# Performance work log

Measured on AMD Instinct MI355X. Metric: run time of the kernel, lower is better.

Reference implementation:

```python
import jax, jax.numpy as jnp
import numpy as np

H = 2048          # hidden_size
I = 1408          # intermediate_size
E = 8             # num_experts
K = 2             # top_k
T = 8192          # tokens


def setup_inputs() -> dict:
    key = jax.random.key(0)
    ks = jax.random.split(key, 7)
    s = 0.02
    return {
        "x": jax.random.normal(ks[0], (T, H), dtype=jnp.float32),
        "w_router": jax.random.normal(ks[1], (H, E), dtype=jnp.float32) * s,
        "w_gate_up": jax.random.normal(ks[2], (E, H, 2 * I), dtype=jnp.float32) * s,
        "w_down": jax.random.normal(ks[3], (E, I, H), dtype=jnp.float32) * s,
        "w_shared_gate_up": jax.random.normal(ks[4], (H, 2 * I), dtype=jnp.float32) * s,
        "w_shared_down": jax.random.normal(ks[5], (I, H), dtype=jnp.float32) * s,
        "w_shared_gate": jax.random.normal(ks[6], (H, 1), dtype=jnp.float32) * s,
    }


def _swiglu_mlp(x, w_gate_up, w_down):
    gu = x @ w_gate_up                      # [T, 2I]
    g, u = jnp.split(gu, 2, axis=-1)
    return (jax.nn.silu(g) * u) @ w_down    # [T, H]


def reference(x, w_router, w_gate_up, w_down, w_shared_gate_up, w_shared_down, w_shared_gate):
    # Router: top-k over logits, softmax over the selected k logits
    logits = x @ w_router                              # [T, E]
    top_vals, top_idx = jax.lax.top_k(logits, K)       # [T, K]
    probs = jax.nn.softmax(top_vals, axis=-1)          # [T, K]

    out = jnp.zeros_like(x)
    for e in range(E):
        sel = (top_idx == e)                           # [T, K] (at most one True per row)
        w_e = jnp.sum(jnp.where(sel, probs, 0.0), axis=-1)  # [T]
        mask = sel.any(axis=-1)                        # [T]
        # Original scales the INPUT by the routing weight before the expert MLP
        xin = x * w_e[:, None]
        o = _swiglu_mlp(xin, w_gate_up[e], w_down[e])
        out = out + jnp.where(mask[:, None], o, 0.0)

    # Shared expert with sigmoid gate
    shared = _swiglu_mlp(x, w_shared_gate_up, w_shared_down)   # [T, H]
    gate = jax.nn.sigmoid(x @ w_shared_gate)                   # [T, 1]
    return out + gate * shared
```

## Files before the change

kernel.cpp:

```cpp
#include <hip/hip_runtime.h>
#include <math.h>

#define H 2048
#define IDIM 1408
#define TWO_I 2816
#define NE 8
#define NTOK 8192
#define BK 32

typedef float f32x4 __attribute__((ext_vector_type(4)));
typedef short bf16x8 __attribute__((ext_vector_type(8)));

#define CNT_OFF   0
#define OFFS_OFF  64
#define BIDX_OFF  1024
#define BW_OFF    (BIDX_OFF + NE*NTOK*4)
#define GATE_OFF  (BW_OFF + NE*NTOK*4)
#define XS_OFF    ((size_t)1 << 20)
#define XS_ROWS   (NTOK + 2*NTOK)
#define WGU_OFF   (XS_OFF  + (size_t)XS_ROWS*H*2)
#define WDN_OFF   (WGU_OFF + (size_t)NE*TWO_I*H*2)
#define WSGU_OFF  (WDN_OFF + (size_t)NE*H*IDIM*2)
#define WSDN_OFF  (WSGU_OFF + (size_t)TWO_I*H*2)
#define ACT_OFF   (WSDN_OFF + (size_t)H*IDIM*2)

#define GLOAD16(g, l) \
    __builtin_amdgcn_global_load_lds((const __attribute__((address_space(1))) void*)(g), \
                                     (__attribute__((address_space(3))) void*)(l), 16, 0, 0)

__device__ inline ushort f2bf(float f) {
    union { float f; uint u; } v; v.f = f;
    uint u = v.u;
    uint r = u + 0x7fffu + ((u >> 16) & 1u);
    return (ushort)(r >> 16);
}

__global__ void zero_meta_kernel(int* p) {
    if (threadIdx.x < 16) p[threadIdx.x] = 0;
}

__global__ void prefix_kernel(const int* __restrict__ cnt, int* __restrict__ offs) {
    if (threadIdx.x == 0) {
        int s = 0;
        for (int e = 0; e < NE; e++) { offs[e] = s; s += cnt[e]; }
    }
}

__global__ __launch_bounds__(64)
void router_kernel(const float* __restrict__ x,
                   const float* __restrict__ w_router,
                   const float* __restrict__ w_sgate,
                   int* __restrict__ cnt,
                   int* __restrict__ bidx,
                   float* __restrict__ bw,
                   float* __restrict__ gate) {
    const int t = blockIdx.x;
    const int lane = threadIdx.x;
    const float* xr = x + (size_t)t * H;

    float acc[NE];
#pragma unroll
    for (int e = 0; e < NE; e++) acc[e] = 0.f;
    float accg = 0.f;

    for (int h = lane; h < H; h += 64) {
        float xv = xr[h];
        const float* wr = w_router + (size_t)h * NE;
#pragma unroll
        for (int e = 0; e < NE; e++) acc[e] += xv * wr[e];
        accg += xv * w_sgate[h];
    }
#pragma unroll
    for (int off = 32; off > 0; off >>= 1) {
#pragma unroll
        for (int e = 0; e < NE; e++) acc[e] += __shfl_down(acc[e], off, 64);
        accg += __shfl_down(accg, off, 64);
    }
    if (lane == 0) {
        int i0 = 0; float v0 = acc[0];
        for (int e = 1; e < NE; e++) if (acc[e] > v0) { v0 = acc[e]; i0 = e; }
        int i1 = -1; float v1 = -3.4e38f;
        for (int e = 0; e < NE; e++) if (e != i0 && acc[e] > v1) { v1 = acc[e]; i1 = e; }
        float e1 = expf(v1 - v0);
        float inv = 1.f / (1.f + e1);
        int pos0 = atomicAdd(&cnt[i0], 1);
        bidx[i0 * NTOK + pos0] = t; bw[i0 * NTOK + pos0] = inv;
        int pos1 = atomicAdd(&cnt[i1], 1);
        bidx[i1 * NTOK + pos1] = t; bw[i1 * NTOK + pos1] = e1 * inv;
        gate[t] = 1.f / (1.f + expf(-accg));
    }
}

__global__ __launch_bounds__(256)
void transpose_cvt(const float* __restrict__ src, ushort* __restrict__ dst, int R, int C) {
    const size_t bs = (size_t)R * C;
    src += (size_t)blockIdx.z * bs;
    dst += (size_t)blockIdx.z * bs;
    const int c0 = blockIdx.x * 64, r0 = blockIdx.y * 64;
    __shared__ float t[64][65];
    const int tid = threadIdx.x;
#pragma unroll
    for (int p = 0; p < 4; p++) {
        int id = tid + p * 256;
        int r = id >> 4, c4 = (id & 15) * 4;
        float4 v = *(const float4*)(src + (size_t)(r0 + r) * C + c0 + c4);
        t[r][c4 + 0] = v.x; t[r][c4 + 1] = v.y; t[r][c4 + 2] = v.z; t[r][c4 + 3] = v.w;
    }
    __syncthreads();
#pragma unroll
    for (int p = 0; p < 4; p++) {
        int id = tid + p * 256;
        int c = id >> 4, r4 = (id & 15) * 4;
        union { ushort us[4]; uint2 v; } o;
#pragma unroll
        for (int q = 0; q < 4; q++) o.us[q] = f2bf(t[r4 + q][c]);
        *(uint2*)(dst + (size_t)(c0 + c) * R + r0 + r4) = o.v;
    }
}

__global__ __launch_bounds__(256)
void xprep_kernel(const float* __restrict__ x, const int* __restrict__ cnt,
                  const int* __restrict__ offs, const int* __restrict__ bidx,
                  const float* __restrict__ bw, ushort* __restrict__ xs) {
    const int y = blockIdx.y;
    const int r = blockIdx.x;
    int srow, drow; float wt;
    if (y == 0) { srow = r; drow = r; wt = 1.f; }
    else {
        int e = y - 1;
        if (r >= cnt[e]) return;
        srow = bidx[e * NTOK + r]; wt = bw[e * NTOK + r];
        drow = NTOK + offs[e] + r;
    }
    const int tid = threadIdx.x;
    const float* sp = x + (size_t)srow * H + tid * 8;
    float4 v0 = *(const float4*)sp;
    float4 v1 = *(const float4*)(sp + 4);
    union { ushort us[8]; uint4 v; } o;
    o.us[0] = f2bf(v0.x * wt); o.us[1] = f2bf(v0.y * wt);
    o.us[2] = f2bf(v0.z * wt); o.us[3] = f2bf(v0.w * wt);
    o.us[4] = f2bf(v1.x * wt); o.us[5] = f2bf(v1.y * wt);
    o.us[6] = f2bf(v1.z * wt); o.us[7] = f2bf(v1.w * wt);
    *(uint4*)(xs + (size_t)drow * H + tid * 8) = o.v;
}

template <bool GATHER>
__global__ __launch_bounds__(256)
void gateup_mfma(const ushort* __restrict__ xs,
                 const ushort* __restrict__ wt,
                 const int* __restrict__ cnt,
                 const int* __restrict__ offs,
                 ushort* __restrict__ act) {
    const int e = GATHER ? blockIdx.z : 0;
    const int rows = GATHER ? cnt[e] : NTOK;
    const int m0 = blockIdx.y * 128;
    if (GATHER && m0 >= rows) return;
    const int n0 = blockIdx.x * 64;
    const ushort* W = wt + (GATHER ? (size_t)e * TWO_I * H : 0);
    const int abase = GATHER ? (NTOK + offs[e]) : 0;
    const int obase = GATHER ? offs[e] : 0;

    __shared__ __align__(16) ushort As[128 * BK];
    __shared__ __align__(16) ushort Bg[64 * BK];
    __shared__ __align__(16) ushort Bu[64 * BK];

    const int tid = threadIdx.x;
    const int wave = tid >> 6, lane = tid & 63;
    const int wm = (wave >> 1) * 64, wn = (wave & 1) * 32;
    const int quad = lane >> 4, l16 = lane & 15;

    const int lr = wave * 16 + (lane >> 2);
    const int lc = (lane & 3) * 8;
    int ga0 = m0 + lr, ga1 = m0 + 64 + lr;
    if (GATHER) {
        if (ga0 >= rows) ga0 = m0;
        if (ga1 >= rows) ga1 = m0;
    }
    const ushort* a0p = xs + (size_t)(abase + ga0) * H + lc;
    const ushort* a1p = xs + (size_t)(abase + ga1) * H + lc;
    const ushort* bgp = W + (size_t)(n0 + lr) * H + lc;
    const ushort* bup = W + (size_t)(IDIM + n0 + lr) * H + lc;
    char* asl0 = (char*)As + wave * 1024;
    char* asl1 = (char*)As + 4096 + wave * 1024;
    char* bgl  = (char*)Bg + wave * 1024;
    char* bul  = (char*)Bu + wave * 1024;

    f32x4 accg[4][2], accu[4][2];
#pragma unroll
    for (int i = 0; i < 4; i++)
#pragma unroll
        for (int j = 0; j < 2; j++) { accg[i][j] = (f32x4)0.f; accu[i][j] = (f32x4)0.f; }

    for (int k0 = 0; k0 < H; k0 += BK) {
        GLOAD16(a0p + k0, asl0);
        GLOAD16(a1p + k0, asl1);
        GLOAD16(bgp + k0, bgl);
        GLOAD16(bup + k0, bul);
        __syncthreads();
        bf16x8 af[4], bgf[2], buf[2];
#pragma unroll
        for (int i = 0; i < 4; i++)
            af[i] = *(const bf16x8*)&As[(wm + i * 16 + l16) * BK + quad * 8];
#pragma unroll
        for (int j = 0; j < 2; j++) {
            bgf[j] = *(const bf16x8*)&Bg[(wn + j * 16 + l16) * BK + quad * 8];
            buf[j] = *(const bf16x8*)&Bu[(wn + j * 16 + l16) * BK + quad * 8];
        }
#pragma unroll
        for (int i = 0; i < 4; i++)
#pragma unroll
            for (int j = 0; j < 2; j++) {
                accg[i][j] = __builtin_amdgcn_mfma_f32_16x16x32_bf16(af[i], bgf[j], accg[i][j], 0, 0, 0);
                accu[i][j] = __builtin_amdgcn_mfma_f32_16x16x32_bf16(af[i], buf[j], accu[i][j], 0, 0, 0);
            }
        __syncthreads();
    }

#pragma unroll
    for (int i = 0; i < 4; i++) {
#pragma unroll
        for (int r = 0; r < 4; r++) {
            int row = m0 + wm + i * 16 + quad * 4 + r;
            if (row >= rows) continue;
            ushort* orow = act + (size_t)(obase + row) * IDIM + n0 + wn + l16;
#pragma unroll
            for (int j = 0; j < 2; j++) {
                float g = accg[i][j][r], u = accu[i][j][r];
                float v = g / (1.f + expf(-g)) * u;
                orow[j * 16] = f2bf(v);
            }
        }
    }
}

template <bool SCATTER>
__global__ __launch_bounds__(256)
void down_mfma(const ushort* __restrict__ act,
               const ushort* __restrict__ wt,
               const int* __restrict__ cnt,
               const int* __restrict__ offs,
               const int* __restrict__ bidx,
               const float* __restrict__ gate,
               float* __restrict__ out) {
    const int e = SCATTER ? blockIdx.z : 0;
    const int rows = SCATTER ? cnt[e] : NTOK;
    const int m0 = blockIdx.y * 128;
    if (SCATTER && m0 >= rows) return;
    const int n0 = blockIdx.x * 128;
    const ushort* W = wt + (SCATTER ? (size_t)e * H * IDIM : 0);
    const ushort* A = act + (size_t)(SCATTER ? offs[e] : 0) * IDIM;

    __shared__ __align__(16) ushort As[128 * BK];
    __shared__ __align__(16) ushort Bs[128 * BK];

    const int tid = threadIdx.x;
    const int wave = tid >> 6, lane = tid & 63;
    const int wm = (wave >> 1) * 64, wn = (wave & 1) * 64;
    const int quad = lane >> 4, l16 = lane & 15;

    const int lr = wave * 16 + (lane >> 2);
    const int lc = (lane & 3) * 8;
    int ga0 = m0 + lr, ga1 = m0 + 64 + lr;
    if (SCATTER) {
        if (ga0 >= rows) ga0 = m0;
        if (ga1 >= rows) ga1 = m0;
    }
    const ushort* a0p = A + (size_t)ga0 * IDIM + lc;
    const ushort* a1p = A + (size_t)ga1 * IDIM + lc;
    const ushort* b0p = W + (size_t)(n0 + lr) * IDIM + lc;
    const ushort* b1p = W + (size_t)(n0 + 64 + lr) * IDIM + lc;
    char* asl0 = (char*)As + wave * 1024;
    char* asl1 = (char*)As + 4096 + wave * 1024;
    char* bsl0 = (char*)Bs + wave * 1024;
    char* bsl1 = (char*)Bs + 4096 + wave * 1024;

    f32x4 acc[4][4];
#pragma unroll
    for (int i = 0; i < 4; i++)
#pragma unroll
        for (int j = 0; j < 4; j++) acc[i][j] = (f32x4)0.f;

    for (int k0 = 0; k0 < IDIM; k0 += BK) {
        GLOAD16(a0p + k0, asl0);
        GLOAD16(a1p + k0, asl1);
        GLOAD16(b0p + k0, bsl0);
        GLOAD16(b1p + k0, bsl1);
        __syncthreads();
        bf16x8 af[4], bf[4];
#pragma unroll
        for (int i = 0; i < 4; i++)
            af[i] = *(const bf16x8*)&As[(wm + i * 16 + l16) * BK + quad * 8];
#pragma unroll
        for (int j = 0; j < 4; j++)
            bf[j] = *(const bf16x8*)&Bs[(wn + j * 16 + l16) * BK + quad * 8];
#pragma unroll
        for (int i = 0; i < 4; i++)
#pragma unroll
            for (int j = 0; j < 4; j++)
                acc[i][j] = __builtin_amdgcn_mfma_f32_16x16x32_bf16(af[i], bf[j], acc[i][j], 0, 0, 0);
        __syncthreads();
    }

#pragma unroll
    for (int i = 0; i < 4; i++) {
#pragma unroll
        for (int r = 0; r < 4; r++) {
            int row = m0 + wm + i * 16 + quad * 4 + r;
            if (row >= rows) continue;
            if (SCATTER) {
                int token = bidx[e * NTOK + row];
                float* orow = out + (size_t)token * H + n0 + wn + l16;
#pragma unroll
                for (int j = 0; j < 4; j++) atomicAdd(&orow[j * 16], acc[i][j][r]);
            } else {
                float gv = gate[row];
                float* orow = out + (size_t)row * H + n0 + wn + l16;
#pragma unroll
                for (int j = 0; j < 4; j++) orow[j * 16] = gv * acc[i][j][r];
            }
        }
    }
}

extern "C" void kernel_launch(void* const* d_in, const int* in_sizes, int n_in,
                              void* d_out, int out_size, void* d_ws, size_t ws_size,
                              hipStream_t stream) {
    const float* x     = (const float*)d_in[0];
    const float* w_rt  = (const float*)d_in[1];
    const float* w_gu  = (const float*)d_in[2];
    const float* w_dn  = (const float*)d_in[3];
    const float* w_sgu = (const float*)d_in[4];
    const float* w_sdn = (const float*)d_in[5];
    const float* w_sg  = (const float*)d_in[6];
    float* out = (float*)d_out;

    char* ws = (char*)d_ws;
    int*    cnt   = (int*)(ws + CNT_OFF);
    int*    offs  = (int*)(ws + OFFS_OFF);
    int*    bidx  = (int*)(ws + BIDX_OFF);
    float*  bw    = (float*)(ws + BW_OFF);
    float*  gate  = (float*)(ws + GATE_OFF);
    ushort* xs    = (ushort*)(ws + XS_OFF);
    ushort* wgu_t = (ushort*)(ws + WGU_OFF);
    ushort* wdn_t = (ushort*)(ws + WDN_OFF);
    ushort* wsgu_t= (ushort*)(ws + WSGU_OFF);
    ushort* wsdn_t= (ushort*)(ws + WSDN_OFF);
    ushort* act   = (ushort*)(ws + ACT_OFF);

    zero_meta_kernel<<<1, 64, 0, stream>>>(cnt);
    router_kernel<<<NTOK, 64, 0, stream>>>(x, w_rt, w_sg, cnt, bidx, bw, gate);
    prefix_kernel<<<1, 64, 0, stream>>>(cnt, offs);

    transpose_cvt<<<dim3(TWO_I / 64, H / 64, NE), 256, 0, stream>>>(w_gu, wgu_t, H, TWO_I);
    transpose_cvt<<<dim3(H / 64, IDIM / 64, NE), 256, 0, stream>>>(w_dn, wdn_t, IDIM, H);
    transpose_cvt<<<dim3(TWO_I / 64, H / 64, 1), 256, 0, stream>>>(w_sgu, wsgu_t, H, TWO_I);
    transpose_cvt<<<dim3(H / 64, IDIM / 64, 1), 256, 0, stream>>>(w_sdn, wsdn_t, IDIM, H);

    xprep_kernel<<<dim3(NTOK, NE + 1), 256, 0, stream>>>(x, cnt, offs, bidx, bw, xs);

    gateup_mfma<false><<<dim3(IDIM / 64, NTOK / 128), 256, 0, stream>>>(xs, wsgu_t, cnt, offs, act);
    down_mfma<false><<<dim3(H / 128, NTOK / 128), 256, 0, stream>>>(act, wsdn_t, cnt, offs, bidx, gate, out);

    gateup_mfma<true><<<dim3(IDIM / 64, NTOK / 128, NE), 256, 0, stream>>>(xs, wgu_t, cnt, offs, act);
    down_mfma<true><<<dim3(H / 128, NTOK / 128, NE), 256, 0, stream>>>(act, wdn_t, cnt, offs, bidx, gate, out);
}
```

Baseline: 1.407 ms.

## Use 256x256 MFMA tiles with a 4-stage swizzled LDS pipeline for the expert GEMMs

Both GEMM kernels move to 512-thread blocks computing 256x256 output tiles. Each keeps a 4-deep ring of LDS buffers, issuing global-to-LDS loads three k-steps ahead and using XOR-swizzled LDS addressing, with setprio placed around the MFMA bursts. The gate/up weights are permuted during the transpose so that gate and up columns sit in interleaved 16-column groups, letting one tile hold both halves for the fused SiLU epilogue. The aim is more data reuse per loaded byte and overlap of memory latency with compute. In exchange it needs 128KB of LDS per block, allowing only one block per CU, and gives coarser grids with more padded work on partially filled expert tiles.

```diff
diff --git a/kernel.cpp b/kernel.cpp
--- a/kernel.cpp
+++ b/kernel.cpp
@@ -28,6 +28,12 @@
     __builtin_amdgcn_global_load_lds((const __attribute__((address_space(1))) void*)(g), \
                                      (__attribute__((address_space(3))) void*)(l), 16, 0, 0)
 
+__device__ inline void wave_barrier() {
+    asm volatile("" ::: "memory");
+    __builtin_amdgcn_s_barrier();
+    asm volatile("" ::: "memory");
+}
+
 __device__ inline ushort f2bf(float f) {
     union { float f; uint u; } v; v.f = f;
     uint u = v.u;
@@ -92,7 +98,7 @@
 }
 
 __global__ __launch_bounds__(256)
-void transpose_cvt(const float* __restrict__ src, ushort* __restrict__ dst, int R, int C) {
+void transpose_cvt(const float* __restrict__ src, ushort* __restrict__ dst, int R, int C, int perm) {
     const size_t bs = (size_t)R * C;
     src += (size_t)blockIdx.z * bs;
     dst += (size_t)blockIdx.z * bs;
@@ -114,7 +120,13 @@
         union { ushort us[4]; uint2 v; } o;
 #pragma unroll
         for (int q = 0; q < 4; q++) o.us[q] = f2bf(t[r4 + q][c]);
-        *(uint2*)(dst + (size_t)(c0 + c) * R + r0 + r4) = o.v;
+        int g = c0 + c;
+        int drow = g;
+        if (perm) {
+            drow = (g < IDIM) ? (((g >> 4) << 5) | (g & 15))
+                              : ((((g - IDIM) >> 4) << 5) | 16 | (g & 15));
+        }
+        *(uint2*)(dst + (size_t)drow * R + r0 + r4) = o.v;
     }
 }
 
@@ -144,8 +156,9 @@
     *(uint4*)(xs + (size_t)drow * H + tid * 8) = o.v;
 }
 
+
 template <bool GATHER>
-__global__ __launch_bounds__(256)
+__global__ __launch_bounds__(512, 2)
 void gateup_mfma(const ushort* __restrict__ xs,
                  const ushort* __restrict__ wt,
                  const int* __restrict__ cnt,
@@ -153,88 +166,110 @@
                  ushort* __restrict__ act) {
     const int e = GATHER ? blockIdx.z : 0;
     const int rows = GATHER ? cnt[e] : NTOK;
-    const int m0 = blockIdx.y * 128;
+    const int m0 = blockIdx.y * 256;
     if (GATHER && m0 >= rows) return;
-    const int n0 = blockIdx.x * 64;
+    const int n0 = blockIdx.x * 256;
     const ushort* W = wt + (GATHER ? (size_t)e * TWO_I * H : 0);
     const int abase = GATHER ? (NTOK + offs[e]) : 0;
     const int obase = GATHER ? offs[e] : 0;
 
-    __shared__ __align__(16) ushort As[128 * BK];
-    __shared__ __align__(16) ushort Bg[64 * BK];
-    __shared__ __align__(16) ushort Bu[64 * BK];
+    __shared__ __align__(16) ushort sA[4 * 8192];
+    __shared__ __align__(16) ushort sB[4 * 8192];
 
     const int tid = threadIdx.x;
-    const int wave = tid >> 6, lane = tid & 63;
-    const int wm = (wave >> 1) * 64, wn = (wave & 1) * 32;
+    const int w = tid >> 6, lane = tid & 63;
+    const int waveM = w >> 2, waveN = w & 3;
     const int quad = lane >> 4, l16 = lane & 15;
 
-    const int lr = wave * 16 + (lane >> 2);
-    const int lc = (lane & 3) * 8;
-    int ga0 = m0 + lr, ga1 = m0 + 64 + lr;
-    if (GATHER) {
-        if (ga0 >= rows) ga0 = m0;
-        if (ga1 >= rows) ga1 = m0;
-    }
-    const ushort* a0p = xs + (size_t)(abase + ga0) * H + lc;
-    const ushort* a1p = xs + (size_t)(abase + ga1) * H + lc;
-    const ushort* bgp = W + (size_t)(n0 + lr) * H + lc;
-    const ushort* bup = W + (size_t)(IDIM + n0 + lr) * H + lc;
-    char* asl0 = (char*)As + wave * 1024;
-    char* asl1 = (char*)As + 4096 + wave * 1024;
-    char* bgl  = (char*)Bg + wave * 1024;
-    char* bul  = (char*)Bu + wave * 1024;
-
-    f32x4 accg[4][2], accu[4][2];
-#pragma unroll
-    for (int i = 0; i < 4; i++)
-#pragma unroll
-        for (int j = 0; j < 2; j++) { accg[i][j] = (f32x4)0.f; accu[i][j] = (f32x4)0.f; }
-
-    for (int k0 = 0; k0 < H; k0 += BK) {
-        GLOAD16(a0p + k0, asl0);
-        GLOAD16(a1p + k0, asl1);
-        GLOAD16(bgp + k0, bgl);
-        GLOAD16(bup + k0, bul);
-        __syncthreads();
-        bf16x8 af[4], bgf[2], buf[2];
-#pragma unroll
-        for (int i = 0; i < 4; i++)
-            af[i] = *(const bf16x8*)&As[(wm + i * 16 + l16) * BK + quad * 8];
-#pragma unroll
-        for (int j = 0; j < 2; j++) {
-            bgf[j] = *(const bf16x8*)&Bg[(wn + j * 16 + l16) * BK + quad * 8];
-            buf[j] = *(const bf16x8*)&Bu[(wn + j * 16 + l16) * BK + quad * 8];
-        }
-#pragma unroll
-        for (int i = 0; i < 4; i++)
-#pragma unroll
-            for (int j = 0; j < 2; j++) {
-                accg[i][j] = __builtin_amdgcn_mfma_f32_16x16x32_bf16(af[i], bgf[j], accg[i][j], 0, 0, 0);
-                accu[i][j] = __builtin_amdgcn_mfma_f32_16x16x32_bf16(af[i], buf[j], accu[i][j], 0, 0, 0);
-            }
-        __syncthreads();
-    }
-
-#pragma unroll
-    for (int i = 0; i < 4; i++) {
-#pragma unroll
-        for (int r = 0; r < 4; r++) {
-            int row = m0 + wm + i * 16 + quad * 4 + r;
-            if (row >= rows) continue;
-            ushort* orow = act + (size_t)(obase + row) * IDIM + n0 + wn + l16;
-#pragma unroll
-            for (int j = 0; j < 2; j++) {
-                float g = accg[i][j][r], u = accu[i][j][r];
-                float v = g / (1.f + expf(-g)) * u;
-                orow[j * 16] = f2bf(v);
+    const int sRow = (w << 4) + (lane >> 2);
+    const int sCol = ((lane & 3) * 8) ^ ((lane >> 5) * 16);
+    int ar0 = m0 + sRow, ar1 = m0 + 128 + sRow;
+    if (GATHER) { int rm = rows - 1; ar0 = min(ar0, rm); ar1 = min(ar1, rm); }
+    const ushort* aG0 = xs + (size_t)(abase + ar0) * H + sCol;
+    const ushort* aG1 = xs + (size_t)(abase + ar1) * H + sCol;
+    const ushort* bG0 = W + (size_t)(n0 + sRow) * H + sCol;
+    const ushort* bG1 = W + (size_t)(n0 + 128 + sRow) * H + sCol;
+
+    const int rdo = l16 * 32 + ((quad * 8) ^ ((l16 >> 3) * 16));
+
+    f32x4 acc[8][4];
+#pragma unroll
+    for (int i = 0; i < 8; i++)
+#pragma unroll
+        for (int j = 0; j < 4; j++) acc[i][j] = (f32x4)0.f;
+
+    const int nkt = H / BK;
+
+#pragma unroll
+    for (int pt = 0; pt < 3; ++pt) {
+        const size_t ko = (size_t)pt * BK;
+        GLOAD16(aG0 + ko, sA + pt * 8192 + w * 512);
+        GLOAD16(aG1 + ko, sA + pt * 8192 + 4096 + w * 512);
+        GLOAD16(bG0 + ko, sB + pt * 8192 + w * 512);
+        GLOAD16(bG1 + ko, sB + pt * 8192 + 4096 + w * 512);
+    }
+    asm volatile("s_waitcnt vmcnt(8)" ::: "memory");
+    wave_barrier();
+
+    for (int t = 0; t < nkt; ++t) {
+        const int bt = t & 3, btS = (t + 3) & 3;
+        const int ktS = (t + 3 < nkt) ? (t + 3) : (nkt - 1);
+        const size_t koS = (size_t)ktS * BK;
+        const ushort* Ab = sA + bt * 8192;
+        const ushort* Bb = sB + bt * 8192;
+
+        bf16x8 fb[4];
+#pragma unroll
+        for (int j = 0; j < 4; ++j)
+            fb[j] = *(const bf16x8*)(Bb + (waveN * 4 + j) * 512 + rdo);
+
+#pragma unroll
+        for (int mh = 0; mh < 2; ++mh) {
+            bf16x8 fa[4];
+#pragma unroll
+            for (int i = 0; i < 4; ++i)
+                fa[i] = *(const bf16x8*)(Ab + (waveM * 8 + mh * 4 + i) * 512 + rdo);
+            __builtin_amdgcn_s_setprio(1);
+#pragma unroll
+            for (int i = 0; i < 4; ++i)
+#pragma unroll
+                for (int j = 0; j < 4; ++j)
+                    acc[mh * 4 + i][j] = __builtin_amdgcn_mfma_f32_16x16x32_bf16(
+                        fa[i], fb[j], acc[mh * 4 + i][j], 0, 0, 0);
+            __builtin_amdgcn_s_setprio(0);
+            if (mh == 0) {
+                GLOAD16(aG0 + koS, sA + btS * 8192 + w * 512);
+                GLOAD16(aG1 + koS, sA + btS * 8192 + 4096 + w * 512);
+            } else {
+                GLOAD16(bG0 + koS, sB + btS * 8192 + w * 512);
+                GLOAD16(bG1 + koS, sB + btS * 8192 + 4096 + w * 512);
             }
         }
+        asm volatile("s_waitcnt vmcnt(8)" ::: "memory");
+        wave_barrier();
+    }
+    asm volatile("s_waitcnt vmcnt(0)" ::: "memory");
+
+    const int icolBase = (n0 + waveN * 64) >> 1;
+#pragma unroll
+    for (int i2 = 0; i2 < 8; ++i2) {
+#pragma unroll
+        for (int r = 0; r < 4; ++r) {
+            int row = m0 + waveM * 128 + i2 * 16 + quad * 4 + r;
+            if (row >= rows) continue;
+            ushort* orow = act + (size_t)(obase + row) * IDIM + icolBase + l16;
+#pragma unroll
+            for (int p = 0; p < 2; ++p) {
+                float g = acc[i2][2 * p][r], u = acc[i2][2 * p + 1][r];
+                float v = g / (1.f + expf(-g)) * u;
+                orow[p * 16] = f2bf(v);
+            }
+        }
     }
 }
 
 template <bool SCATTER>
-__global__ __launch_bounds__(256)
+__global__ __launch_bounds__(512, 2)
 void down_mfma(const ushort* __restrict__ act,
                const ushort* __restrict__ wt,
                const int* __restrict__ cnt,
@@ -244,79 +279,105 @@
                float* __restrict__ out) {
     const int e = SCATTER ? blockIdx.z : 0;
     const int rows = SCATTER ? cnt[e] : NTOK;
-    const int m0 = blockIdx.y * 128;
+    const int m0 = blockIdx.y * 256;
     if (SCATTER && m0 >= rows) return;
-    const int n0 = blockIdx.x * 128;
+    const int n0 = blockIdx.x * 256;
     const ushort* W = wt + (SCATTER ? (size_t)e * H * IDIM : 0);
     const ushort* A = act + (size_t)(SCATTER ? offs[e] : 0) * IDIM;
 
-    __shared__ __align__(16) ushort As[128 * BK];
-    __shared__ __align__(16) ushort Bs[128 * BK];
+    __shared__ __align__(16) ushort sA[4 * 8192];
+    __shared__ __align__(16) ushort sB[4 * 8192];
 
     const int tid = threadIdx.x;
-    const int wave = tid >> 6, lane = tid & 63;
-    const int wm = (wave >> 1) * 64, wn = (wave & 1) * 64;
+    const int w = tid >> 6, lane = tid & 63;
+    const int waveM = w >> 2, waveN = w & 3;
     const int quad = lane >> 4, l16 = lane & 15;
 
-    const int lr = wave * 16 + (lane >> 2);
-    const int lc = (lane & 3) * 8;
-    int ga0 = m0 + lr, ga1 = m0 + 64 + lr;
-    if (SCATTER) {
-        if (ga0 >= rows) ga0 = m0;
-        if (ga1 >= rows) ga1 = m0;
-    }
-    const ushort* a0p = A + (size_t)ga0 * IDIM + lc;
-    const ushort* a1p = A + (size_t)ga1 * IDIM + lc;
-    const ushort* b0p = W + (size_t)(n0 + lr) * IDIM + lc;
-    const ushort* b1p = W + (size_t)(n0 + 64 + lr) * IDIM + lc;
-    char* asl0 = (char*)As + wave * 1024;
-    char* asl1 = (char*)As + 4096 + wave * 1024;
-    char* bsl0 = (char*)Bs + wave * 1024;
-    char* bsl1 = (char*)Bs + 4096 + wave * 1024;
-
-    f32x4 acc[4][4];
-#pragma unroll
-    for (int i = 0; i < 4; i++)
+    const int sRow = (w << 4) + (lane >> 2);
+    const int sCol = ((lane & 3) * 8) ^ ((lane >> 5) * 16);
+    int ar0 = m0 + sRow, ar1 = m0 + 128 + sRow;
+    if (SCATTER) { int rm = rows - 1; ar0 = min(ar0, rm); ar1 = min(ar1, rm); }
+    const ushort* aG0 = A + (size_t)ar0 * IDIM + sCol;
+    const ushort* aG1 = A + (size_t)ar1 * IDIM + sCol;
+    const ushort* bG0 = W + (size_t)(n0 + sRow) * IDIM + sCol;
+    const ushort* bG1 = W + (size_t)(n0 + 128 + sRow) * IDIM + sCol;
+
+    const int rdo = l16 * 32 + ((quad * 8) ^ ((l16 >> 3) * 16));
+
+    f32x4 acc[8][4];
+#pragma unroll
+    for (int i = 0; i < 8; i++)
 #pragma unroll
         for (int j = 0; j < 4; j++) acc[i][j] = (f32x4)0.f;
 
-    for (int k0 = 0; k0 < IDIM; k0 += BK) {
-        GLOAD16(a0p + k0, asl0);
-        GLOAD16(a1p + k0, asl1);
-        GLOAD16(b0p + k0, bsl0);
-        GLOAD16(b1p + k0, bsl1);
-        __syncthreads();
-        bf16x8 af[4], bf[4];
-#pragma unroll
-        for (int i = 0; i < 4; i++)
-            af[i] = *(const bf16x8*)&As[(wm + i * 16 + l16) * BK + quad * 8];
-#pragma unroll
-        for (int j = 0; j < 4; j++)
-            bf[j] = *(const bf16x8*)&Bs[(wn + j * 16 + l16) * BK + quad * 8];
-#pragma unroll
-        for (int i = 0; i < 4; i++)
-#pragma unroll
-            for (int j = 0; j < 4; j++)
-                acc[i][j] = __builtin_amdgcn_mfma_f32_16x16x32_bf16(af[i], bf[j], acc[i][j], 0, 0, 0);
-        __syncthreads();
-    }
-
-#pragma unroll
-    for (int i = 0; i < 4; i++) {
-#pragma unroll
-        for (int r = 0; r < 4; r++) {
-            int row = m0 + wm + i * 16 + quad * 4 + r;
+    const int nkt = IDIM / BK;
+
+#pragma unroll
+    for (int pt = 0; pt < 3; ++pt) {
+        const size_t ko = (size_t)pt * BK;
+        GLOAD16(aG0 + ko, sA + pt * 8192 + w * 512);
+        GLOAD16(aG1 + ko, sA + pt * 8192 + 4096 + w * 512);
+        GLOAD16(bG0 + ko, sB + pt * 8192 + w * 512);
+        GLOAD16(bG1 + ko, sB + pt * 8192 + 4096 + w * 512);
+    }
+    asm volatile("s_waitcnt vmcnt(8)" ::: "memory");
+    wave_barrier();
+
+    for (int t = 0; t < nkt; ++t) {
+        const int bt = t & 3, btS = (t + 3) & 3;
+        const int ktS = (t + 3 < nkt) ? (t + 3) : (nkt - 1);
+        const size_t koS = (size_t)ktS * BK;
+        const ushort* Ab = sA + bt * 8192;
+        const ushort* Bb = sB + bt * 8192;
+
+        bf16x8 fb[4];
+#pragma unroll
+        for (int j = 0; j < 4; ++j)
+            fb[j] = *(const bf16x8*)(Bb + (waveN * 4 + j) * 512 + rdo);
+
+#pragma unroll
+        for (int mh = 0; mh < 2; ++mh) {
+            bf16x8 fa[4];
+#pragma unroll
+            for (int i = 0; i < 4; ++i)
+                fa[i] = *(const bf16x8*)(Ab + (waveM * 8 + mh * 4 + i) * 512 + rdo);
+            __builtin_amdgcn_s_setprio(1);
+#pragma unroll
+            for (int i = 0; i < 4; ++i)
+#pragma unroll
+                for (int j = 0; j < 4; ++j)
+                    acc[mh * 4 + i][j] = __builtin_amdgcn_mfma_f32_16x16x32_bf16(
+                        fa[i], fb[j], acc[mh * 4 + i][j], 0, 0, 0);
+            __builtin_amdgcn_s_setprio(0);
+            if (mh == 0) {
+                GLOAD16(aG0 + koS, sA + btS * 8192 + w * 512);
+                GLOAD16(aG1 + koS, sA + btS * 8192 + 4096 + w * 512);
+            } else {
+                GLOAD16(bG0 + koS, sB + btS * 8192 + w * 512);
+                GLOAD16(bG1 + koS, sB + btS * 8192 + 4096 + w * 512);
+            }
+        }
+        asm volatile("s_waitcnt vmcnt(8)" ::: "memory");
+        wave_barrier();
+    }
+    asm volatile("s_waitcnt vmcnt(0)" ::: "memory");
+
+#pragma unroll
+    for (int i2 = 0; i2 < 8; ++i2) {
+#pragma unroll
+        for (int r = 0; r < 4; ++r) {
+            int row = m0 + waveM * 128 + i2 * 16 + quad * 4 + r;
             if (row >= rows) continue;
             if (SCATTER) {
                 int token = bidx[e * NTOK + row];
-                float* orow = out + (size_t)token * H + n0 + wn + l16;
-#pragma unroll
-                for (int j = 0; j < 4; j++) atomicAdd(&orow[j * 16], acc[i][j][r]);
+                float* orow = out + (size_t)token * H + n0 + waveN * 64 + l16;
+#pragma unroll
+                for (int j = 0; j < 4; ++j) atomicAdd(&orow[j * 16], acc[i2][j][r]);
             } else {
                 float gv = gate[row];
-                float* orow = out + (size_t)row * H + n0 + wn + l16;
-#pragma unroll
-                for (int j = 0; j < 4; j++) orow[j * 16] = gv * acc[i][j][r];
+                float* orow = out + (size_t)row * H + n0 + waveN * 64 + l16;
+#pragma unroll
+                for (int j = 0; j < 4; ++j) orow[j * 16] = gv * acc[i2][j][r];
             }
         }
     }
@@ -351,16 +412,16 @@
     router_kernel<<<NTOK, 64, 0, stream>>>(x, w_rt, w_sg, cnt, bidx, bw, gate);
     prefix_kernel<<<1, 64, 0, stream>>>(cnt, offs);
 
-    transpose_cvt<<<dim3(TWO_I / 64, H / 64, NE), 256, 0, stream>>>(w_gu, wgu_t, H, TWO_I);
-    transpose_cvt<<<dim3(H / 64, IDIM / 64, NE), 256, 0, stream>>>(w_dn, wdn_t, IDIM, H);
-    transpose_cvt<<<dim3(TWO_I / 64, H / 64, 1), 256, 0, stream>>>(w_sgu, wsgu_t, H, TWO_I);
-    transpose_cvt<<<dim3(H / 64, IDIM / 64, 1), 256, 0, stream>>>(w_sdn, wsdn_t, IDIM, H);
+    transpose_cvt<<<dim3(TWO_I / 64, H / 64, NE), 256, 0, stream>>>(w_gu, wgu_t, H, TWO_I, 1);
+    transpose_cvt<<<dim3(H / 64, IDIM / 64, NE), 256, 0, stream>>>(w_dn, wdn_t, IDIM, H, 0);
+    transpose_cvt<<<dim3(TWO_I / 64, H / 64, 1), 256, 0, stream>>>(w_sgu, wsgu_t, H, TWO_I, 1);
+    transpose_cvt<<<dim3(H / 64, IDIM / 64, 1), 256, 0, stream>>>(w_sdn, wsdn_t, IDIM, H, 0);
 
     xprep_kernel<<<dim3(NTOK, NE + 1), 256, 0, stream>>>(x, cnt, offs, bidx, bw, xs);
 
-    gateup_mfma<false><<<dim3(IDIM / 64, NTOK / 128), 256, 0, stream>>>(xs, wsgu_t, cnt, offs, act);
-    down_mfma<false><<<dim3(H / 128, NTOK / 128), 256, 0, stream>>>(act, wsdn_t, cnt, offs, bidx, gate, out);
-
-    gateup_mfma<true><<<dim3(IDIM / 64, NTOK / 128, NE), 256, 0, stream>>>(xs, wgu_t, cnt, offs, act);
-    down_mfma<true><<<dim3(H / 128, NTOK / 128, NE), 256, 0, stream>>>(act, wdn_t, cnt, offs, bidx, gate, out);
-}
+    gateup_mfma<false><<<dim3(TWO_I / 256, NTOK / 256), 512, 0, stream>>>(xs, wsgu_t, cnt, offs, act);
+    down_mfma<false><<<dim3(H / 256, NTOK / 256), 512, 0, stream>>>(act, wsdn_t, cnt, offs, bidx, gate, out);
+
+    gateup_mfma<true><<<dim3(TWO_I / 256, NTOK / 256, NE), 512, 0, stream>>>(xs, wgu_t, cnt, offs, act);
+    down_mfma<true><<<dim3(H / 256, NTOK / 256, NE), 512, 0, stream>>>(act, wdn_t, cnt, offs, bidx, gate, out);
+}
```

New measurement: 1.383 ms. About the same (-1.7%).
